# Kernel tuning notes

Measured on AMD Instinct MI355X. Metric: run time of the kernel, lower is better.

The kernel has to match this reference:

```python
import jax, jax.numpy as jnp
import numpy as np

L, D, H, HD, FF, V = 6, 768, 12, 64, 3072, 2051
NUM_SEM, NUM_AC = 1024, 1024
TEMP = 1.0


def _ln(x, g, b):
    m = jnp.mean(x, axis=-1, keepdims=True)
    v = jnp.mean((x - m) ** 2, axis=-1, keepdims=True)
    return (x - m) / jnp.sqrt(v + 1e-5) * g + b


def _gpt2_logits(tokens, pos, wte, wpe, layer_params, lnf_g, lnf_b):
    # tokens, pos: [B, T]
    B, T = tokens.shape
    h = wte[tokens] + wpe[pos]
    causal = jnp.tril(jnp.ones((T, T), dtype=bool))

    def blk(h, p):
        ln1g, ln1b, aw, ab, pw, pb, ln2g, ln2b, fw, fb, fpw, fpb = p
        x = _ln(h, ln1g, ln1b)
        qkv = x @ aw + ab                       # [B, T, 3D]
        q, k, v = jnp.split(qkv, 3, axis=-1)
        q = q.reshape(B, T, H, HD)
        k = k.reshape(B, T, H, HD)
        v = v.reshape(B, T, H, HD)
        s = jnp.einsum('bqhd,bkhd->bhqk', q, k) / jnp.sqrt(jnp.float32(HD))
        s = jnp.where(causal, s, -jnp.inf)
        a = jax.nn.softmax(s, axis=-1)
        o = jnp.einsum('bhqk,bkhd->bqhd', a, v).reshape(B, T, D)
        h = h + o @ pw + pb
        x2 = _ln(h, ln2g, ln2b)
        h = h + jax.nn.gelu(x2 @ fw + fb, approximate=True) @ fpw + fpb
        return h, None

    h, _ = jax.lax.scan(blk, h, layer_params)
    h = _ln(h, lnf_g, lnf_b)
    return h @ wte.T                            # tied LM head: [B, T, V]


def setup_inputs() -> dict:
    key = jax.random.key(0)
    ks = jax.random.split(key, 12)
    s = 0.02
    inp = {
        'wte': jax.random.normal(ks[0], (V, D)) * s,
        'wpe': jax.random.normal(ks[1], (1024, D)) * s,
        'ln1_g': jnp.ones((L, D)), 'ln1_b': jnp.zeros((L, D)),
        'attn_w': jax.random.normal(ks[2], (L, D, 3 * D)) * s,
        'attn_b': jnp.zeros((L, 3 * D)),
        'proj_w': jax.random.normal(ks[3], (L, D, D)) * s,
        'proj_b': jnp.zeros((L, D)),
        'ln2_g': jnp.ones((L, D)), 'ln2_b': jnp.zeros((L, D)),
        'fc_w': jax.random.normal(ks[4], (L, D, FF)) * s,
        'fc_b': jnp.zeros((L, FF)),
        'fcp_w': jax.random.normal(ks[5], (L, FF, D)) * s,
        'fcp_b': jnp.zeros((L, D)),
        'lnf_g': jnp.ones((D,)), 'lnf_b': jnp.zeros((D,)),
        'first_idx': jax.random.randint(ks[6], (1, 128), 0, V).astype(jnp.int32),
        'pos_ids': jnp.arange(128, dtype=jnp.int32)[None, :],
        'max_len': 16,
        'topk': 64,
    }
    return inp


def reference(wte, wpe, ln1_g, ln1_b, attn_w, attn_b, proj_w, proj_b,
              ln2_g, ln2_b, fc_w, fc_b, fcp_w, fcp_b, lnf_g, lnf_b,
              first_idx, pos_ids, max_len, topk):
    B, P = first_idx.shape
    layer_params = (ln1_g, ln1_b, attn_w, attn_b, proj_w, proj_b,
                    ln2_g, ln2_b, fc_w, fc_b, fcp_w, fcp_b)
    # static-shape buffers: prompt + max_len decode slots (full-seq recompute/step)
    pos_full = jnp.concatenate(
        [pos_ids, pos_ids[:, -1:] + 1 + jnp.arange(max_len, dtype=pos_ids.dtype)[None, :]], axis=1)
    idx_buf = jnp.concatenate([first_idx, jnp.zeros((B, max_len), first_idx.dtype)], axis=1)
    keys = jax.random.split(jax.random.key(1), max_len)
    band = jnp.arange(V)
    inf_mask = (band <= NUM_SEM) | (band == NUM_SEM + 1 + NUM_AC)
    kk = min(topk, V)

    def step(carry, k):
        buf, cur = carry
        logits_full = _gpt2_logits(buf, pos_full, wte, wpe, layer_params, lnf_g, lnf_b)
        logits = jax.lax.dynamic_slice_in_dim(logits_full, cur - 1, 1, axis=1)[:, 0, :]
        logits = logits * TEMP
        logits = jnp.where(inf_mask[None, :], -jnp.inf, logits)
        v, _ = jax.lax.top_k(logits, kk)
        logits = jnp.where(logits < v[:, -1:], -jnp.inf, logits)
        samp = jax.random.categorical(k, logits).astype(buf.dtype)
        buf = jax.lax.dynamic_update_slice(buf, samp[:, None], (jnp.int32(0), cur))
        return (buf, cur + 1), logits

    (idx_buf, _), step_logits = jax.lax.scan(step, (idx_buf, jnp.int32(P)), keys)
    return idx_buf, step_logits
```

## Files before the change

kernel.cpp:

```cpp
#include <hip/hip_runtime.h>
#include <cstdint>
#include <cstddef>

#define DD 768
#define DD3 2304
#define NH 12
#define HDIM 64
#define FFD 3072
#define VV 2051
#define NL 6
#define PLEN 128
#define TMAX 144
#define NSTEP 16
#define KTOP 64
#define NEG_BIG (-3.0e38f)

__host__ __device__ __forceinline__ uint32_t rotl32(uint32_t x, int r){
  return (x << r) | (x >> (32 - r));
}
__host__ __device__ __forceinline__ void threefry2x32(uint32_t k0, uint32_t k1,
    uint32_t x0, uint32_t x1, uint32_t& o0, uint32_t& o1){
  uint32_t ks2 = k0 ^ k1 ^ 0x1BD11BDAu;
  x0 += k0; x1 += k1;
  #define TFR(r) { x0 += x1; x1 = rotl32(x1, r); x1 ^= x0; }
  TFR(13) TFR(15) TFR(26) TFR(6)
  x0 += k1;  x1 += ks2 + 1u;
  TFR(17) TFR(29) TFR(16) TFR(24)
  x0 += ks2; x1 += k0 + 2u;
  TFR(13) TFR(15) TFR(26) TFR(6)
  x0 += k0;  x1 += k1 + 3u;
  TFR(17) TFR(29) TFR(16) TFR(24)
  x0 += k1;  x1 += ks2 + 4u;
  TFR(13) TFR(15) TFR(26) TFR(6)
  x0 += ks2; x1 += k0 + 5u;
  #undef TFR
  o0 = x0; o1 = x1;
}

__device__ __forceinline__ float gumbel_for(uint32_t ka, uint32_t kb, int j){
  uint32_t i  = (j < 1026) ? (uint32_t)j : (uint32_t)(j - 1026);
  uint32_t x1 = 1026u + i;
  uint32_t o0, o1; threefry2x32(ka, kb, i, x1, o0, o1);
  uint32_t bits = (j < 1026) ? o0 : o1;
  uint32_t fb = (bits >> 9) | 0x3f800000u;
  float u = __uint_as_float(fb) - 1.0f;
  const float TINY = 1.17549435e-38f;
  if (u < TINY) u = TINY;
  return -logf(-logf(u));
}

__device__ __forceinline__ float gelu_f(float x){
  float x3 = x * x * x;
  return 0.5f * x * (1.0f + tanhf(0.7978845608028654f * (x + 0.044715f * x3)));
}

__device__ __forceinline__ void ln_stats(const float* hs, float* red, int tid,
                                         float& m, float& rs){
  float s = 0.f, q = 0.f;
  for (int d = tid; d < DD; d += 256){ float v = hs[d]; s += v; q += v * v; }
  red[tid] = s; red[256 + tid] = q; __syncthreads();
  for (int st = 128; st > 0; st >>= 1){
    if (tid < st){ red[tid] += red[tid + st]; red[256 + tid] += red[256 + tid + st]; }
    __syncthreads();
  }
  m = red[0] * (1.0f / DD);
  float var = red[256] * (1.0f / DD) - m * m;
  rs = 1.0f / sqrtf(var + 1e-5f);
  __syncthreads();
}

__global__ void k_init(const int* __restrict__ fidx, float* __restrict__ dout,
                       int* __restrict__ tok, float* __restrict__ zb){
  int tid = threadIdx.x;
  for (int i = tid; i < PLEN; i += 256){ int t = fidx[i]; tok[i] = t; dout[i] = (float)t; }
  for (int d = tid; d < DD; d += 256) zb[d] = 0.0f;
}

__global__ void k_embed_pref(const int* __restrict__ tok, const float* __restrict__ wte,
                             const float* __restrict__ wpe, float* __restrict__ h){
  int t = blockIdx.x, tid = threadIdx.x;
  int tk = tok[t];
  for (int d = tid; d < DD; d += 256)
    h[t * DD + d] = wte[(size_t)tk * DD + d] + wpe[(size_t)t * DD + d];
}

__global__ __launch_bounds__(1024) void k_embed_dec(const int* __restrict__ tok,
    const float* __restrict__ wte, const float* __restrict__ wpe,
    float* __restrict__ hM, float* __restrict__ hP, float* __restrict__ qkvd, int p){
  int tid = threadIdx.x;
  int tk = tok[p];
  if (tid < DD){
    hM[tid] = wte[(size_t)tk * DD + tid] + wpe[(size_t)p * DD + tid];
    hP[tid] = 0.0f;
  }
  for (int j = tid; j < DD3; j += 1024) qkvd[j] = 0.0f;
}

__global__ __launch_bounds__(256) void k_ln(const float* __restrict__ in, float* __restrict__ out,
                     const float* __restrict__ g, const float* __restrict__ b){
  __shared__ float hs[DD]; __shared__ float red[512];
  int r = blockIdx.x, tid = threadIdx.x;
  const float* x = in + (size_t)r * DD;
  for (int d = tid; d < DD; d += 256) hs[d] = x[d];
  __syncthreads();
  float m, rs; ln_stats(hs, red, tid, m, rs);
  for (int d = tid; d < DD; d += 256) out[(size_t)r * DD + d] = (hs[d] - m) * rs * g[d] + b[d];
}

template<int ACT, int ACC>
__global__ __launch_bounds__(256) void k_gemm(const float* __restrict__ A, const float* __restrict__ B,
                       const float* __restrict__ bias, float* __restrict__ C,
                       int M, int N, int K){
  __shared__ float As[64][17];
  __shared__ float Bs[16][68];
  int tid = threadIdx.x;
  int tx = tid & 15, ty = tid >> 4;
  int n0 = blockIdx.x * 64, m0 = blockIdx.y * 64;
  float acc[4][4] = {};
  for (int k0 = 0; k0 < K; k0 += 16){
    {
      int r = tid >> 2, c4 = (tid & 3) * 4;
      float4 v = *reinterpret_cast<const float4*>(A + (size_t)(m0 + r) * K + k0 + c4);
      As[r][c4] = v.x; As[r][c4 + 1] = v.y; As[r][c4 + 2] = v.z; As[r][c4 + 3] = v.w;
    }
    {
      int r = tid >> 4, c4 = (tid & 15) * 4;
      float4 v = *reinterpret_cast<const float4*>(B + (size_t)(k0 + r) * N + n0 + c4);
      Bs[r][c4] = v.x; Bs[r][c4 + 1] = v.y; Bs[r][c4 + 2] = v.z; Bs[r][c4 + 3] = v.w;
    }
    __syncthreads();
    #pragma unroll
    for (int kk = 0; kk < 16; kk++){
      float a[4], bb[4];
      #pragma unroll
      for (int r = 0; r < 4; r++) a[r] = As[ty * 4 + r][kk];
      #pragma unroll
      for (int c = 0; c < 4; c++) bb[c] = Bs[kk][tx * 4 + c];
      #pragma unroll
      for (int r = 0; r < 4; r++)
        #pragma unroll
        for (int c = 0; c < 4; c++) acc[r][c] += a[r] * bb[c];
    }
    __syncthreads();
  }
  #pragma unroll
  for (int r = 0; r < 4; r++){
    int mi = m0 + ty * 4 + r;
    #pragma unroll
    for (int c = 0; c < 4; c++){
      int ni = n0 + tx * 4 + c;
      float v = acc[r][c] + bias[ni];
      if (ACC) v += C[(size_t)mi * N + ni];
      if (ACT) v = gelu_f(v);
      C[(size_t)mi * N + ni] = v;
    }
  }
}

__global__ void k_kvcopy(const float* __restrict__ qkvb, float* __restrict__ kc,
                         float* __restrict__ vc){
  int t = blockIdx.x, tid = threadIdx.x;
  for (int d = tid; d < DD; d += 256){
    kc[(size_t)t * DD + d] = qkvb[(size_t)t * DD3 + DD + d];
    vc[(size_t)t * DD + d] = qkvb[(size_t)t * DD3 + 2 * DD + d];
  }
}

__global__ __launch_bounds__(128) void k_attn_pref(const float* __restrict__ qkvb,
    const float* __restrict__ kc, const float* __restrict__ vc, float* __restrict__ attno){
  int h = blockIdx.x, t = blockIdx.y, tid = threadIdx.x;
  __shared__ float q[HDIM]; __shared__ float sc[PLEN];
  __shared__ float mxs, sms;
  if (tid < HDIM) q[tid] = qkvb[(size_t)t * DD3 + h * HDIM + tid];
  __syncthreads();
  if (tid <= t){
    const float* kr = kc + (size_t)tid * DD + h * HDIM;
    float a = 0.f;
    #pragma unroll
    for (int d = 0; d < HDIM; d++) a += q[d] * kr[d];
    sc[tid] = a * 0.125f;
  }
  __syncthreads();
  if (tid == 0){ float mx = -INFINITY; for (int j = 0; j <= t; j++) mx = fmaxf(mx, sc[j]); mxs = mx; }
  __syncthreads();
  if (tid <= t) sc[tid] = expf(sc[tid] - mxs);
  __syncthreads();
  if (tid == 0){ float s = 0.f; for (int j = 0; j <= t; j++) s += sc[j]; sms = 1.0f / s; }
  __syncthreads();
  if (tid < HDIM){
    float acc = 0.f;
    for (int j = 0; j <= t; j++) acc += sc[j] * vc[(size_t)j * DD + h * HDIM + tid];
    attno[(size_t)t * DD + h * HDIM + tid] = acc * sms;
  }
}

__global__ __launch_bounds__(256) void k_dec_qkv(const float* __restrict__ hMin,
    const float* __restrict__ hP, float* __restrict__ hMout,
    const float* __restrict__ g, const float* __restrict__ b,
    const float* __restrict__ aw, const float* __restrict__ ab, float* __restrict__ qkvd){
  __shared__ float hs[DD]; __shared__ float red[512];
  int tid = threadIdx.x, blk = blockIdx.x;
  int jt = blk % 9, ds = blk / 9;
  for (int d = tid; d < DD; d += 256) hs[d] = hMin[d] + hP[d];
  __syncthreads();
  float m, rs; ln_stats(hs, red, tid, m, rs);
  if (blk < 3) hMout[blk * 256 + tid] = hs[blk * 256 + tid];
  int j = jt * 256 + tid;
  float acc = (ds == 0) ? ab[j] : 0.0f;
  int d0 = ds * 32;
  #pragma unroll 4
  for (int dd = 0; dd < 32; dd++){
    int d = d0 + dd;
    float xd = (hs[d] - m) * rs * g[d] + b[d];
    acc += xd * aw[(size_t)d * DD3 + j];
  }
  atomicAdd(&qkvd[j], acc);
}

__global__ __launch_bounds__(256) void k_dec_attn(const float* __restrict__ qkvd,
    float* __restrict__ kc, float* __restrict__ vc, float* __restrict__ hMout,
    const float* __restrict__ pw, const float* __restrict__ pb,
    float* __restrict__ hP, float* __restrict__ ffpre, int p){
  int blk = blockIdx.x; int h = blk >> 2, es = blk & 3;
  int tid = threadIdx.x;
  __shared__ float q[HDIM]; __shared__ float sc[TMAX]; __shared__ float o[HDIM];
  __shared__ float mxs, sms;
  if (tid < HDIM){
    float kk = qkvd[DD + h * HDIM + tid];
    float vv = qkvd[2 * DD + h * HDIM + tid];
    kc[(size_t)p * DD + h * HDIM + tid] = kk;
    vc[(size_t)p * DD + h * HDIM + tid] = vv;
    q[tid] = qkvd[h * HDIM + tid];
  }
  if (es == 0 && tid < HDIM) hP[h * HDIM + tid] = 0.0f;
  if (tid < HDIM) ffpre[blk * HDIM + tid] = 0.0f;
  __syncthreads();
  for (int j = tid; j <= p; j += 256){
    const float* kr = kc + (size_t)j * DD + h * HDIM;
    float a = 0.f;
    #pragma unroll
    for (int d = 0; d < HDIM; d++) a += q[d] * kr[d];
    sc[j] = a * 0.125f;
  }
  __syncthreads();
  if (tid == 0){ float mx = -INFINITY; for (int j = 0; j <= p; j++) mx = fmaxf(mx, sc[j]); mxs = mx; }
  __syncthreads();
  for (int j = tid; j <= p; j += 256) sc[j] = expf(sc[j] - mxs);
  __syncthreads();
  if (tid == 0){ float s = 0.f; for (int j = 0; j <= p; j++) s += sc[j]; sms = 1.0f / s; }
  __syncthreads();
  if (tid < HDIM){
    float acc = 0.f;
    for (int j = 0; j <= p; j++) acc += sc[j] * vc[(size_t)j * DD + h * HDIM + tid];
    o[tid] = acc * sms;
  }
  __syncthreads();
  for (int dd = tid; dd < 192; dd += 256){
    int dout = es * 192 + dd;
    float acc = (h == 0) ? pb[dout] : 0.0f;
    const float* pwb = pw + (size_t)(h * HDIM) * DD + dout;
    #pragma unroll 8
    for (int e = 0; e < HDIM; e++) acc += o[e] * pwb[(size_t)e * DD];
    atomicAdd(&hMout[dout], acc);
  }
}

__global__ __launch_bounds__(256) void k_dec_fc(const float* __restrict__ hM,
    const float* __restrict__ g, const float* __restrict__ b,
    const float* __restrict__ fw, float* __restrict__ ffpre, float* __restrict__ qkvd_zero){
  __shared__ float hs[DD]; __shared__ float red[512];
  int tid = threadIdx.x, blk = blockIdx.x;
  int jt = blk % 12, ds = blk / 12;
  for (int d = tid; d < DD; d += 256) hs[d] = hM[d];
  __syncthreads();
  float m, rs; ln_stats(hs, red, tid, m, rs);
  if (blk < 9) qkvd_zero[blk * 256 + tid] = 0.0f;
  int j = jt * 256 + tid;
  float acc = 0.f;
  int d0 = ds * 48;
  #pragma unroll 4
  for (int dd = 0; dd < 48; dd++){
    int d = d0 + dd;
    float xd = (hs[d] - m) * rs * g[d] + b[d];
    acc += xd * fw[(size_t)d * FFD + j];
  }
  atomicAdd(&ffpre[j], acc);
}

__global__ __launch_bounds__(256) void k_dec_fcp(const float* __restrict__ ffpre,
    const float* __restrict__ fb, const float* __restrict__ fcpw,
    const float* __restrict__ fpb, float* __restrict__ hP){
  __shared__ float gv[16];
  int tid = threadIdx.x, blk = blockIdx.x;
  int j0 = blk * 16;
  if (tid < 16) gv[tid] = gelu_f(ffpre[j0 + tid] + fb[j0 + tid]);
  __syncthreads();
  float a0 = 0.f, a1 = 0.f, a2 = 0.f;
  for (int jj = 0; jj < 16; jj++){
    const float* row = fcpw + (size_t)(j0 + jj) * DD;
    float gj = gv[jj];
    a0 += gj * row[tid];
    a1 += gj * row[tid + 256];
    a2 += gj * row[tid + 512];
  }
  if (blk == 0){ a0 += fpb[tid]; a1 += fpb[tid + 256]; a2 += fpb[tid + 512]; }
  atomicAdd(&hP[tid], a0);
  atomicAdd(&hP[tid + 256], a1);
  atomicAdd(&hP[tid + 512], a2);
}

__global__ __launch_bounds__(256) void k_logits(const float* __restrict__ hM,
    const float* __restrict__ hP, const float* __restrict__ g, const float* __restrict__ b,
    const float* __restrict__ wte, float* __restrict__ lg){
  __shared__ float xf[DD]; __shared__ float red[512];
  int tid = threadIdx.x;
  for (int d = tid; d < DD; d += 256) xf[d] = hM[d] + hP[d];
  __syncthreads();
  float m, rs; ln_stats(xf, red, tid, m, rs);
  for (int d = tid; d < DD; d += 256) xf[d] = (xf[d] - m) * rs * g[d] + b[d];
  __syncthreads();
  int w = tid >> 6, lane = tid & 63;
  int j = blockIdx.x * 4 + w;
  if (j < VV){
    const float* wr = wte + (size_t)j * DD;
    float acc = 0.f;
    #pragma unroll
    for (int it = 0; it < DD / 64; it++){ int d = lane + it * 64; acc += xf[d] * wr[d]; }
    #pragma unroll
    for (int off = 32; off > 0; off >>= 1) acc += __shfl_down(acc, off);
    if (lane == 0) lg[j] = acc;
  }
}

__global__ __launch_bounds__(1024) void k_sample(const float* __restrict__ lg,
    float* __restrict__ dout, int* __restrict__ tok, int step, int cur,
    uint32_t ka, uint32_t kb){
  __shared__ float lv[VV];
  __shared__ unsigned int hist[256];
  __shared__ unsigned int sprefix; __shared__ int srem;
  __shared__ float bz[1024]; __shared__ int bi[1024];
  int tid = threadIdx.x;
  for (int j = tid; j < VV; j += 1024){
    float x = lg[j] * 1.0f;
    if (j <= 1024 || j == 2049) x = -INFINITY;
    lv[j] = x;
  }
  if (tid == 0){ sprefix = 0u; srem = KTOP; }
  __syncthreads();
  for (int pass = 0; pass < 4; pass++){
    if (tid < 256) hist[tid] = 0u;
    __syncthreads();
    int shift = 24 - 8 * pass;
    unsigned int pref = sprefix;
    for (int j = tid; j < VV; j += 1024){
      unsigned int bits = __float_as_uint(lv[j]);
      unsigned int u = (bits & 0x80000000u) ? ~bits : (bits | 0x80000000u);
      bool ok = (pass == 0) || ((u >> (shift + 8)) == pref);
      if (ok) atomicAdd(&hist[(u >> shift) & 255u], 1u);
    }
    __syncthreads();
    if (tid == 0){
      int rem = srem; unsigned int cum = 0; int bin = 0;
      for (int bnum = 255; bnum >= 0; bnum--){
        unsigned int c = hist[bnum];
        if (cum + c >= (unsigned int)rem){ bin = bnum; srem = rem - (int)cum; break; }
        cum += c;
      }
      sprefix = (pref << 8) | (unsigned int)bin;
    }
    __syncthreads();
  }
  unsigned int tu = sprefix;
  float T = __uint_as_float((tu & 0x80000000u) ? (tu ^ 0x80000000u) : ~tu);
  for (int j = tid; j < VV; j += 1024){
    float x = lv[j];
    if (x < T) x = -INFINITY;
    lv[j] = x;
    dout[TMAX + (size_t)step * VV + j] = (x == -INFINITY) ? NEG_BIG : x;
  }
  __syncthreads();
  float best = -INFINITY; int besti = 0x7fffffff;
  for (int j = tid; j < VV; j += 1024){
    float gg = gumbel_for(ka, kb, j);
    float z = lv[j] + gg;
    if (z > best){ best = z; besti = j; }
  }
  bz[tid] = best; bi[tid] = besti; __syncthreads();
  for (int st = 512; st > 0; st >>= 1){
    if (tid < st){
      if (bz[tid + st] > bz[tid] || (bz[tid + st] == bz[tid] && bi[tid + st] < bi[tid])){
        bz[tid] = bz[tid + st]; bi[tid] = bi[tid + st];
      }
    }
    __syncthreads();
  }
  if (tid == 0){ tok[cur] = bi[0]; dout[cur] = (float)bi[0]; }
}

extern "C" void kernel_launch(void* const* d_in, const int* in_sizes, int n_in,
                              void* d_out, int out_size, void* d_ws, size_t ws_size,
                              hipStream_t stream){
  const float* wte  = (const float*)d_in[0];
  const float* wpe  = (const float*)d_in[1];
  const float* ln1g = (const float*)d_in[2];
  const float* ln1b = (const float*)d_in[3];
  const float* aw   = (const float*)d_in[4];
  const float* ab   = (const float*)d_in[5];
  const float* pw   = (const float*)d_in[6];
  const float* pb   = (const float*)d_in[7];
  const float* ln2g = (const float*)d_in[8];
  const float* ln2b = (const float*)d_in[9];
  const float* fw   = (const float*)d_in[10];
  const float* fb   = (const float*)d_in[11];
  const float* fcpw = (const float*)d_in[12];
  const float* fpb  = (const float*)d_in[13];
  const float* lnfg = (const float*)d_in[14];
  const float* lnfb = (const float*)d_in[15];
  const int*   fidx = (const int*)d_in[16];
  float* dout = (float*)d_out;

  float* ws = (float*)d_ws;
  size_t off = 0;
  auto alloc = [&](size_t n){ float* pp = ws + off; off += (n + 255) & ~(size_t)255; return pp; };
  float* h      = alloc((size_t)PLEN * DD);
  float* xln    = alloc((size_t)PLEN * DD);
  float* qkvb   = alloc((size_t)PLEN * DD3);
  float* attno  = alloc((size_t)PLEN * DD);
  float* ffb    = alloc((size_t)PLEN * FFD);
  float* kcache = alloc((size_t)NL * TMAX * DD);
  float* vcache = alloc((size_t)NL * TMAX * DD);
  float* hM0 = alloc(DD); float* hM1 = alloc(DD); float* hP = alloc(DD);
  float* zb  = alloc(DD);
  float* qkvd  = alloc(DD3);
  float* ffpre = alloc(FFD);
  float* lgb   = alloc(VV);
  int*   tok   = (int*)alloc(256);

  uint32_t keys[NSTEP][2];
  {
    uint32_t y0[16], y1[16];
    for (int i = 0; i < 16; i++) threefry2x32(0u, 1u, (uint32_t)i, (uint32_t)(16 + i), y0[i], y1[i]);
    uint32_t outk[32];
    for (int i = 0; i < 16; i++){ outk[i] = y0[i]; outk[16 + i] = y1[i]; }
    for (int j = 0; j < 16; j++){ keys[j][0] = outk[2 * j]; keys[j][1] = outk[2 * j + 1]; }
  }

  k_init<<<1, 256, 0, stream>>>(fidx, dout, tok, zb);
  k_embed_pref<<<PLEN, 256, 0, stream>>>(tok, wte, wpe, h);
  for (int l = 0; l < NL; l++){
    float* kc = kcache + (size_t)l * TMAX * DD;
    float* vc = vcache + (size_t)l * TMAX * DD;
    k_ln<<<PLEN, 256, 0, stream>>>(h, xln, ln1g + l * DD, ln1b + l * DD);
    k_gemm<0,0><<<dim3(DD3 / 64, PLEN / 64), 256, 0, stream>>>(
        xln, aw + (size_t)l * DD * DD3, ab + (size_t)l * DD3, qkvb, PLEN, DD3, DD);
    k_kvcopy<<<PLEN, 256, 0, stream>>>(qkvb, kc, vc);
    k_attn_pref<<<dim3(NH, PLEN), 128, 0, stream>>>(qkvb, kc, vc, attno);
    k_gemm<0,1><<<dim3(DD / 64, PLEN / 64), 256, 0, stream>>>(
        attno, pw + (size_t)l * DD * DD, pb + (size_t)l * DD, h, PLEN, DD, DD);
    k_ln<<<PLEN, 256, 0, stream>>>(h, xln, ln2g + l * DD, ln2b + l * DD);
    k_gemm<1,0><<<dim3(FFD / 64, PLEN / 64), 256, 0, stream>>>(
        xln, fw + (size_t)l * DD * FFD, fb + (size_t)l * FFD, ffb, PLEN, FFD, DD);
    k_gemm<0,1><<<dim3(DD / 64, PLEN / 64), 256, 0, stream>>>(
        ffb, fcpw + (size_t)l * FFD * DD, fpb + (size_t)l * DD, h, PLEN, DD, FFD);
  }
  k_logits<<<513, 256, 0, stream>>>(h + (size_t)(PLEN - 1) * DD, zb, lnfg, lnfb, wte, lgb);
  k_sample<<<1, 1024, 0, stream>>>(lgb, dout, tok, 0, PLEN, keys[0][0], keys[0][1]);

  for (int i = 1; i < NSTEP; i++){
    int p = PLEN - 1 + i;
    k_embed_dec<<<1, 1024, 0, stream>>>(tok, wte, wpe, hM0, hP, qkvd, p);
    for (int l = 0; l < NL; l++){
      float* hin  = (l & 1) ? hM1 : hM0;
      float* hout = (l & 1) ? hM0 : hM1;
      float* kc = kcache + (size_t)l * TMAX * DD;
      float* vc = vcache + (size_t)l * TMAX * DD;
      k_dec_qkv<<<216, 256, 0, stream>>>(hin, hP, hout,
          ln1g + l * DD, ln1b + l * DD,
          aw + (size_t)l * DD * DD3, ab + (size_t)l * DD3, qkvd);
      k_dec_attn<<<48, 256, 0, stream>>>(qkvd, kc, vc, hout,
          pw + (size_t)l * DD * DD, pb + (size_t)l * DD, hP, ffpre, p);
      k_dec_fc<<<192, 256, 0, stream>>>(hout, ln2g + l * DD, ln2b + l * DD,
          fw + (size_t)l * DD * FFD, ffpre, qkvd);
      k_dec_fcp<<<192, 256, 0, stream>>>(ffpre, fb + (size_t)l * FFD,
          fcpw + (size_t)l * FFD * DD, fpb + (size_t)l * DD, hP);
    }
    k_logits<<<513, 256, 0, stream>>>(hM0, hP, lnfg, lnfb, wte, lgb);
    k_sample<<<1, 1024, 0, stream>>>(lgb, dout, tok, i, PLEN + i, keys[i][0], keys[i][1]);
  }
}
```

Before: 7.761 ms.

## Fuse per-step decode kernels into one persistent kernel with grid barriers

Replaces the ~27 kernel launches per decode step (embed, per-layer qkv/attn/fc/fcp, logits, sample) with a single 256-block persistent kernel that separates stages with a software global barrier built on atomics. Buffer zeroing is folded into idle blocks of earlier stages, and the sampling stage is reimplemented with 256 threads. This removes launch overhead and inter-kernel gaps in the latency-bound decode loop. The cost is spin-wait barriers, which assume all 256 blocks are co-resident, and lower parallelism in the logits stage.

```diff
diff --git a/kernel.cpp b/kernel.cpp
--- a/kernel.cpp
+++ b/kernel.cpp
@@ -69,11 +69,31 @@
   __syncthreads();
 }
 
+__device__ __forceinline__ void gbar(int* cnt, int* gen){
+  __syncthreads();
+  if (threadIdx.x == 0){
+    __threadfence();
+    int g = atomicAdd(gen, 0);
+    if (atomicAdd(cnt, 1) == 255){
+      atomicExch(cnt, 0);
+      __threadfence();
+      atomicAdd(gen, 1);
+    } else {
+      while (atomicAdd(gen, 0) == g) __builtin_amdgcn_s_sleep(1);
+    }
+  }
+  __syncthreads();
+  __threadfence();
+}
+
 __global__ void k_init(const int* __restrict__ fidx, float* __restrict__ dout,
-                       int* __restrict__ tok, float* __restrict__ zb){
+                       int* __restrict__ tok, float* __restrict__ zb,
+                       float* __restrict__ qkvd, int* __restrict__ bar){
   int tid = threadIdx.x;
   for (int i = tid; i < PLEN; i += 256){ int t = fidx[i]; tok[i] = t; dout[i] = (float)t; }
   for (int d = tid; d < DD; d += 256) zb[d] = 0.0f;
+  for (int j = tid; j < DD3; j += 256) qkvd[j] = 0.0f;
+  if (tid < 2) bar[tid] = 0;
 }
 
 __global__ void k_embed_pref(const int* __restrict__ tok, const float* __restrict__ wte,
@@ -82,18 +102,6 @@
   int tk = tok[t];
   for (int d = tid; d < DD; d += 256)
     h[t * DD + d] = wte[(size_t)tk * DD + d] + wpe[(size_t)t * DD + d];
-}
-
-__global__ __launch_bounds__(1024) void k_embed_dec(const int* __restrict__ tok,
-    const float* __restrict__ wte, const float* __restrict__ wpe,
-    float* __restrict__ hM, float* __restrict__ hP, float* __restrict__ qkvd, int p){
-  int tid = threadIdx.x;
-  int tk = tok[p];
-  if (tid < DD){
-    hM[tid] = wte[(size_t)tk * DD + tid] + wpe[(size_t)p * DD + tid];
-    hP[tid] = 0.0f;
-  }
-  for (int j = tid; j < DD3; j += 1024) qkvd[j] = 0.0f;
 }
 
 __global__ __launch_bounds__(256) void k_ln(const float* __restrict__ in, float* __restrict__ out,
@@ -194,121 +202,6 @@
   }
 }
 
-__global__ __launch_bounds__(256) void k_dec_qkv(const float* __restrict__ hMin,
-    const float* __restrict__ hP, float* __restrict__ hMout,
-    const float* __restrict__ g, const float* __restrict__ b,
-    const float* __restrict__ aw, const float* __restrict__ ab, float* __restrict__ qkvd){
-  __shared__ float hs[DD]; __shared__ float red[512];
-  int tid = threadIdx.x, blk = blockIdx.x;
-  int jt = blk % 9, ds = blk / 9;
-  for (int d = tid; d < DD; d += 256) hs[d] = hMin[d] + hP[d];
-  __syncthreads();
-  float m, rs; ln_stats(hs, red, tid, m, rs);
-  if (blk < 3) hMout[blk * 256 + tid] = hs[blk * 256 + tid];
-  int j = jt * 256 + tid;
-  float acc = (ds == 0) ? ab[j] : 0.0f;
-  int d0 = ds * 32;
-  #pragma unroll 4
-  for (int dd = 0; dd < 32; dd++){
-    int d = d0 + dd;
-    float xd = (hs[d] - m) * rs * g[d] + b[d];
-    acc += xd * aw[(size_t)d * DD3 + j];
-  }
-  atomicAdd(&qkvd[j], acc);
-}
-
-__global__ __launch_bounds__(256) void k_dec_attn(const float* __restrict__ qkvd,
-    float* __restrict__ kc, float* __restrict__ vc, float* __restrict__ hMout,
-    const float* __restrict__ pw, const float* __restrict__ pb,
-    float* __restrict__ hP, float* __restrict__ ffpre, int p){
-  int blk = blockIdx.x; int h = blk >> 2, es = blk & 3;
-  int tid = threadIdx.x;
-  __shared__ float q[HDIM]; __shared__ float sc[TMAX]; __shared__ float o[HDIM];
-  __shared__ float mxs, sms;
-  if (tid < HDIM){
-    float kk = qkvd[DD + h * HDIM + tid];
-    float vv = qkvd[2 * DD + h * HDIM + tid];
-    kc[(size_t)p * DD + h * HDIM + tid] = kk;
-    vc[(size_t)p * DD + h * HDIM + tid] = vv;
-    q[tid] = qkvd[h * HDIM + tid];
-  }
-  if (es == 0 && tid < HDIM) hP[h * HDIM + tid] = 0.0f;
-  if (tid < HDIM) ffpre[blk * HDIM + tid] = 0.0f;
-  __syncthreads();
-  for (int j = tid; j <= p; j += 256){
-    const float* kr = kc + (size_t)j * DD + h * HDIM;
-    float a = 0.f;
-    #pragma unroll
-    for (int d = 0; d < HDIM; d++) a += q[d] * kr[d];
-    sc[j] = a * 0.125f;
-  }
-  __syncthreads();
-  if (tid == 0){ float mx = -INFINITY; for (int j = 0; j <= p; j++) mx = fmaxf(mx, sc[j]); mxs = mx; }
-  __syncthreads();
-  for (int j = tid; j <= p; j += 256) sc[j] = expf(sc[j] - mxs);
-  __syncthreads();
-  if (tid == 0){ float s = 0.f; for (int j = 0; j <= p; j++) s += sc[j]; sms = 1.0f / s; }
-  __syncthreads();
-  if (tid < HDIM){
-    float acc = 0.f;
-    for (int j = 0; j <= p; j++) acc += sc[j] * vc[(size_t)j * DD + h * HDIM + tid];
-    o[tid] = acc * sms;
-  }
-  __syncthreads();
-  for (int dd = tid; dd < 192; dd += 256){
-    int dout = es * 192 + dd;
-    float acc = (h == 0) ? pb[dout] : 0.0f;
-    const float* pwb = pw + (size_t)(h * HDIM) * DD + dout;
-    #pragma unroll 8
-    for (int e = 0; e < HDIM; e++) acc += o[e] * pwb[(size_t)e * DD];
-    atomicAdd(&hMout[dout], acc);
-  }
-}
-
-__global__ __launch_bounds__(256) void k_dec_fc(const float* __restrict__ hM,
-    const float* __restrict__ g, const float* __restrict__ b,
-    const float* __restrict__ fw, float* __restrict__ ffpre, float* __restrict__ qkvd_zero){
-  __shared__ float hs[DD]; __shared__ float red[512];
-  int tid = threadIdx.x, blk = blockIdx.x;
-  int jt = blk % 12, ds = blk / 12;
-  for (int d = tid; d < DD; d += 256) hs[d] = hM[d];
-  __syncthreads();
-  float m, rs; ln_stats(hs, red, tid, m, rs);
-  if (blk < 9) qkvd_zero[blk * 256 + tid] = 0.0f;
-  int j = jt * 256 + tid;
-  float acc = 0.f;
-  int d0 = ds * 48;
-  #pragma unroll 4
-  for (int dd = 0; dd < 48; dd++){
-    int d = d0 + dd;
-    float xd = (hs[d] - m) * rs * g[d] + b[d];
-    acc += xd * fw[(size_t)d * FFD + j];
-  }
-  atomicAdd(&ffpre[j], acc);
-}
-
-__global__ __launch_bounds__(256) void k_dec_fcp(const float* __restrict__ ffpre,
-    const float* __restrict__ fb, const float* __restrict__ fcpw,
-    const float* __restrict__ fpb, float* __restrict__ hP){
-  __shared__ float gv[16];
-  int tid = threadIdx.x, blk = blockIdx.x;
-  int j0 = blk * 16;
-  if (tid < 16) gv[tid] = gelu_f(ffpre[j0 + tid] + fb[j0 + tid]);
-  __syncthreads();
-  float a0 = 0.f, a1 = 0.f, a2 = 0.f;
-  for (int jj = 0; jj < 16; jj++){
-    const float* row = fcpw + (size_t)(j0 + jj) * DD;
-    float gj = gv[jj];
-    a0 += gj * row[tid];
-    a1 += gj * row[tid + 256];
-    a2 += gj * row[tid + 512];
-  }
-  if (blk == 0){ a0 += fpb[tid]; a1 += fpb[tid + 256]; a2 += fpb[tid + 512]; }
-  atomicAdd(&hP[tid], a0);
-  atomicAdd(&hP[tid + 256], a1);
-  atomicAdd(&hP[tid + 512], a2);
-}
-
 __global__ __launch_bounds__(256) void k_logits(const float* __restrict__ hM,
     const float* __restrict__ hP, const float* __restrict__ g, const float* __restrict__ b,
     const float* __restrict__ wte, float* __restrict__ lg){
@@ -341,7 +234,7 @@
   __shared__ float bz[1024]; __shared__ int bi[1024];
   int tid = threadIdx.x;
   for (int j = tid; j < VV; j += 1024){
-    float x = lg[j] * 1.0f;
+    float x = lg[j];
     if (j <= 1024 || j == 2049) x = -INFINITY;
     lv[j] = x;
   }
@@ -395,6 +288,249 @@
     __syncthreads();
   }
   if (tid == 0){ tok[cur] = bi[0]; dout[cur] = (float)bi[0]; }
+}
+
+__global__ __launch_bounds__(256) void k_decode_step(
+    const float* __restrict__ wte, const float* __restrict__ wpe,
+    const float* __restrict__ ln1g, const float* __restrict__ ln1b,
+    const float* __restrict__ aw, const float* __restrict__ ab,
+    const float* __restrict__ pw, const float* __restrict__ pb,
+    const float* __restrict__ ln2g, const float* __restrict__ ln2b,
+    const float* __restrict__ fw, const float* __restrict__ fb,
+    const float* __restrict__ fcpw, const float* __restrict__ fpb,
+    const float* __restrict__ lnfg, const float* __restrict__ lnfb,
+    float* __restrict__ hM0, float* __restrict__ hM1, float* __restrict__ hP,
+    float* __restrict__ qkvd, float* __restrict__ ffpre,
+    float* __restrict__ kcache, float* __restrict__ vcache,
+    float* __restrict__ lgb, int* __restrict__ tok, float* __restrict__ dout,
+    int* __restrict__ bar, int stepi, int p,
+    uint32_t ka, uint32_t kb){
+  __shared__ __align__(16) char smem_raw[11520];
+  int tid = threadIdx.x, bid = blockIdx.x;
+  int* bcnt = bar; int* bgen = bar + 1;
+  float* hout = hM0;
+
+  for (int l = 0; l < NL; l++){
+    const float* hin = (l & 1) ? hM1 : hM0;
+    hout = (l & 1) ? hM0 : hM1;
+    float* kc = kcache + (size_t)l * TMAX * DD;
+    float* vc = vcache + (size_t)l * TMAX * DD;
+    const float* g1 = ln1g + l * DD; const float* b1 = ln1b + l * DD;
+    const float* awl = aw + (size_t)l * DD * DD3; const float* abl = ab + (size_t)l * DD3;
+    const float* pwl = pw + (size_t)l * DD * DD;  const float* pbl = pb + (size_t)l * DD;
+    const float* g2 = ln2g + l * DD; const float* b2 = ln2b + l * DD;
+    const float* fwl = fw + (size_t)l * DD * FFD; const float* fbl = fb + (size_t)l * FFD;
+    const float* fcpl = fcpw + (size_t)l * FFD * DD; const float* fpbl = fpb + (size_t)l * DD;
+
+    {
+      float* hs = (float*)smem_raw; float* red = hs + DD;
+      if (bid < 216){
+        if (l == 0){
+          int tk = tok[p];
+          for (int d = tid; d < DD; d += 256)
+            hs[d] = wte[(size_t)tk * DD + d] + wpe[(size_t)p * DD + d];
+        } else {
+          for (int d = tid; d < DD; d += 256) hs[d] = hin[d] + hP[d];
+        }
+        __syncthreads();
+        float m, rs; ln_stats(hs, red, tid, m, rs);
+        if (bid < 3) hout[bid * 256 + tid] = hs[bid * 256 + tid];
+        int jt = bid % 9, ds = bid / 9;
+        int j = jt * 256 + tid;
+        float acc = (ds == 0) ? abl[j] : 0.0f;
+        int d0 = ds * 32;
+        #pragma unroll 4
+        for (int dd = 0; dd < 32; dd++){
+          int d = d0 + dd;
+          float xd = (hs[d] - m) * rs * g1[d] + b1[d];
+          acc += xd * awl[(size_t)d * DD3 + j];
+        }
+        atomicAdd(&qkvd[j], acc);
+      } else if (bid < 228){
+        ffpre[(bid - 216) * 256 + tid] = 0.0f;
+      }
+      gbar(bcnt, bgen);
+    }
+
+    {
+      if (bid < 48){
+        int h = bid >> 2, es = bid & 3;
+        float* q = (float*)smem_raw; float* sc = q + HDIM; float* o = sc + TMAX;
+        float* mxp = o + HDIM; float* smp = mxp + 1;
+        if (tid < HDIM){
+          float kk = qkvd[DD + h * HDIM + tid];
+          float vv = qkvd[2 * DD + h * HDIM + tid];
+          kc[(size_t)p * DD + h * HDIM + tid] = kk;
+          vc[(size_t)p * DD + h * HDIM + tid] = vv;
+          q[tid] = qkvd[h * HDIM + tid];
+        }
+        __syncthreads();
+        for (int j = tid; j <= p; j += 256){
+          const float* kr = kc + (size_t)j * DD + h * HDIM;
+          float a = 0.f;
+          #pragma unroll
+          for (int d = 0; d < HDIM; d++) a += q[d] * kr[d];
+          sc[j] = a * 0.125f;
+        }
+        __syncthreads();
+        if (tid == 0){ float mx = -INFINITY; for (int j = 0; j <= p; j++) mx = fmaxf(mx, sc[j]); *mxp = mx; }
+        __syncthreads();
+        float mxs = *mxp;
+        for (int j = tid; j <= p; j += 256) sc[j] = expf(sc[j] - mxs);
+        __syncthreads();
+        if (tid == 0){ float s = 0.f; for (int j = 0; j <= p; j++) s += sc[j]; *smp = 1.0f / s; }
+        __syncthreads();
+        float sms = *smp;
+        if (tid < HDIM){
+          float acc = 0.f;
+          for (int j = 0; j <= p; j++) acc += sc[j] * vc[(size_t)j * DD + h * HDIM + tid];
+          o[tid] = acc * sms;
+        }
+        __syncthreads();
+        for (int dd = tid; dd < 192; dd += 256){
+          int dout_ = es * 192 + dd;
+          float acc = (h == 0) ? pbl[dout_] : 0.0f;
+          const float* pwb = pwl + (size_t)(h * HDIM) * DD + dout_;
+          #pragma unroll 8
+          for (int e = 0; e < HDIM; e++) acc += o[e] * pwb[(size_t)e * DD];
+          atomicAdd(&hout[dout_], acc);
+        }
+      } else if (bid < 51){
+        hP[(bid - 48) * 256 + tid] = 0.0f;
+      }
+      gbar(bcnt, bgen);
+    }
+
+    {
+      float* hs = (float*)smem_raw; float* red = hs + DD;
+      if (bid < 192){
+        for (int d = tid; d < DD; d += 256) hs[d] = hout[d];
+        __syncthreads();
+        float m, rs; ln_stats(hs, red, tid, m, rs);
+        int jt = bid % 12, ds = bid / 12;
+        int j = jt * 256 + tid;
+        float acc = 0.f;
+        int d0 = ds * 48;
+        #pragma unroll 4
+        for (int dd = 0; dd < 48; dd++){
+          int d = d0 + dd;
+          float xd = (hs[d] - m) * rs * g2[d] + b2[d];
+          acc += xd * fwl[(size_t)d * FFD + j];
+        }
+        atomicAdd(&ffpre[j], acc);
+      } else if (bid < 201){
+        qkvd[(bid - 192) * 256 + tid] = 0.0f;
+      }
+      gbar(bcnt, bgen);
+    }
+
+    {
+      if (bid < 192){
+        float* gv = (float*)smem_raw;
+        int j0 = bid * 16;
+        if (tid < 16) gv[tid] = gelu_f(ffpre[j0 + tid] + fbl[j0 + tid]);
+        __syncthreads();
+        float a0 = 0.f, a1 = 0.f, a2 = 0.f;
+        for (int jj = 0; jj < 16; jj++){
+          const float* row = fcpl + (size_t)(j0 + jj) * DD;
+          float gj = gv[jj];
+          a0 += gj * row[tid];
+          a1 += gj * row[tid + 256];
+          a2 += gj * row[tid + 512];
+        }
+        if (bid == 0){ a0 += fpbl[tid]; a1 += fpbl[tid + 256]; a2 += fpbl[tid + 512]; }
+        atomicAdd(&hP[tid], a0);
+        atomicAdd(&hP[tid + 256], a1);
+        atomicAdd(&hP[tid + 512], a2);
+      }
+      gbar(bcnt, bgen);
+    }
+  }
+
+  {
+    float* xf = (float*)smem_raw; float* red = xf + DD;
+    for (int d = tid; d < DD; d += 256) xf[d] = hout[d] + hP[d];
+    __syncthreads();
+    float m, rs; ln_stats(xf, red, tid, m, rs);
+    for (int d = tid; d < DD; d += 256) xf[d] = (xf[d] - m) * rs * lnfg[d] + lnfb[d];
+    __syncthreads();
+    int w = tid >> 6, lane = tid & 63;
+    int jend = (bid == 255) ? VV : bid * 8 + 8;
+    for (int j = bid * 8 + w; j < jend; j += 4){
+      const float* wr = wte + (size_t)j * DD;
+      float acc = 0.f;
+      #pragma unroll
+      for (int it = 0; it < DD / 64; it++){ int d = lane + it * 64; acc += xf[d] * wr[d]; }
+      #pragma unroll
+      for (int off = 32; off > 0; off >>= 1) acc += __shfl_down(acc, off);
+      if (lane == 0) lgb[j] = acc;
+    }
+    gbar(bcnt, bgen);
+  }
+
+  if (bid == 0){
+    float* lv = (float*)smem_raw;
+    unsigned int* hist = (unsigned int*)(lv + VV);
+    float* bz = (float*)(hist + 256);
+    int* bi = (int*)(bz + 256);
+    volatile unsigned int* sprefix = (volatile unsigned int*)(bi + 256);
+    volatile int* srem = (volatile int*)(sprefix + 1);
+    for (int j = tid; j < VV; j += 256){
+      float x = lgb[j];
+      if (j <= 1024 || j == 2049) x = -INFINITY;
+      lv[j] = x;
+    }
+    if (tid == 0){ *sprefix = 0u; *srem = KTOP; }
+    __syncthreads();
+    for (int pass = 0; pass < 4; pass++){
+      if (tid < 256) hist[tid] = 0u;
+      __syncthreads();
+      int shift = 24 - 8 * pass;
+      unsigned int pref = *sprefix;
+      for (int j = tid; j < VV; j += 256){
+        unsigned int bits = __float_as_uint(lv[j]);
+        unsigned int u = (bits & 0x80000000u) ? ~bits : (bits | 0x80000000u);
+        bool ok = (pass == 0) || ((u >> (shift + 8)) == pref);
+        if (ok) atomicAdd(&hist[(u >> shift) & 255u], 1u);
+      }
+      __syncthreads();
+      if (tid == 0){
+        int rem = *srem; unsigned int cum = 0; int bin = 0;
+        for (int bnum = 255; bnum >= 0; bnum--){
+          unsigned int c = hist[bnum];
+          if (cum + c >= (unsigned int)rem){ bin = bnum; *srem = rem - (int)cum; break; }
+          cum += c;
+        }
+        *sprefix = (pref << 8) | (unsigned int)bin;
+      }
+      __syncthreads();
+    }
+    unsigned int tu = *sprefix;
+    float T = __uint_as_float((tu & 0x80000000u) ? (tu ^ 0x80000000u) : ~tu);
+    for (int j = tid; j < VV; j += 256){
+      float x = lv[j];
+      if (x < T) x = -INFINITY;
+      lv[j] = x;
+      dout[TMAX + (size_t)stepi * VV + j] = (x == -INFINITY) ? NEG_BIG : x;
+    }
+    __syncthreads();
+    float best = -INFINITY; int besti = 0x7fffffff;
+    for (int j = tid; j < VV; j += 256){
+      float gg = gumbel_for(ka, kb, j);
+      float z = lv[j] + gg;
+      if (z > best){ best = z; besti = j; }
+    }
+    bz[tid] = best; bi[tid] = besti; __syncthreads();
+    for (int st = 128; st > 0; st >>= 1){
+      if (tid < st){
+        if (bz[tid + st] > bz[tid] || (bz[tid + st] == bz[tid] && bi[tid + st] < bi[tid])){
+          bz[tid] = bz[tid + st]; bi[tid] = bi[tid + st];
+        }
+      }
+      __syncthreads();
+    }
+    if (tid == 0){ tok[p + 1] = bi[0]; dout[p + 1] = (float)bi[0]; }
+  }
 }
 
 extern "C" void kernel_launch(void* const* d_in, const int* in_sizes, int n_in,
@@ -435,6 +571,7 @@
   float* ffpre = alloc(FFD);
   float* lgb   = alloc(VV);
   int*   tok   = (int*)alloc(256);
+  int*   bar   = (int*)alloc(64);
 
   uint32_t keys[NSTEP][2];
   {
@@ -445,7 +582,7 @@
     for (int j = 0; j < 16; j++){ keys[j][0] = outk[2 * j]; keys[j][1] = outk[2 * j + 1]; }
   }
 
-  k_init<<<1, 256, 0, stream>>>(fidx, dout, tok, zb);
+  k_init<<<1, 256, 0, stream>>>(fidx, dout, tok, zb, qkvd, bar);
   k_embed_pref<<<PLEN, 256, 0, stream>>>(tok, wte, wpe, h);
   for (int l = 0; l < NL; l++){
     float* kc = kcache + (size_t)l * TMAX * DD;
@@ -468,23 +605,10 @@
 
   for (int i = 1; i < NSTEP; i++){
     int p = PLEN - 1 + i;
-    k_embed_dec<<<1, 1024, 0, stream>>>(tok, wte, wpe, hM0, hP, qkvd, p);
-    for (int l = 0; l < NL; l++){
-      float* hin  = (l & 1) ? hM1 : hM0;
-      float* hout = (l & 1) ? hM0 : hM1;
-      float* kc = kcache + (size_t)l * TMAX * DD;
-      float* vc = vcache + (size_t)l * TMAX * DD;
-      k_dec_qkv<<<216, 256, 0, stream>>>(hin, hP, hout,
-          ln1g + l * DD, ln1b + l * DD,
-          aw + (size_t)l * DD * DD3, ab + (size_t)l * DD3, qkvd);
-      k_dec_attn<<<48, 256, 0, stream>>>(qkvd, kc, vc, hout,
-          pw + (size_t)l * DD * DD, pb + (size_t)l * DD, hP, ffpre, p);
-      k_dec_fc<<<192, 256, 0, stream>>>(hout, ln2g + l * DD, ln2b + l * DD,
-          fw + (size_t)l * DD * FFD, ffpre, qkvd);
-      k_dec_fcp<<<192, 256, 0, stream>>>(ffpre, fb + (size_t)l * FFD,
-          fcpw + (size_t)l * FFD * DD, fpb + (size_t)l * DD, hP);
-    }
-    k_logits<<<513, 256, 0, stream>>>(hM0, hP, lnfg, lnfb, wte, lgb);
-    k_sample<<<1, 1024, 0, stream>>>(lgb, dout, tok, i, PLEN + i, keys[i][0], keys[i][1]);
-  }
-}
+    k_decode_step<<<256, 256, 0, stream>>>(
+        wte, wpe, ln1g, ln1b, aw, ab, pw, pb, ln2g, ln2b,
+        fw, fb, fcpw, fpb, lnfg, lnfb,
+        hM0, hM1, hP, qkvd, ffpre, kcache, vcache,
+        lgb, tok, dout, bar, i, p, keys[i][0], keys[i][1]);
+  }
+}
```

Measured after the change: 19.64 ms. +153.1%, slower.
